# Optimization experiments

Measured on AMD Instinct MI355X. Metric: run time of the kernel, lower is better.

Reference implementation:

```python
import jax, jax.numpy as jnp
import numpy as np

N = 4096  # num_dev == num_task (required by elementwise msg computation)
D = 64    # embed_dim


def setup_inputs() -> dict:
    key = jax.random.key(0)
    ks = jax.random.split(key, 10)
    return {
        "embed": jax.random.normal(ks[0], (2 * N, D), jnp.float32),
        "adj_collab": jnp.zeros((N, N), jnp.float32),   # only .shape[0] is used
        "adj_interact": jnp.zeros((N, N), jnp.float32),  # unused in forward body
        "adj_similar": jnp.zeros((N, N), jnp.float32),   # unused in forward body
        "collab_score": jax.random.normal(ks[1], (N, N), jnp.float32),
        "interact_score": jax.random.normal(ks[2], (N, N), jnp.float32),
        "similar_score": jax.random.normal(ks[3], (N, N), jnp.float32),
        "deg_dev": jax.random.uniform(ks[4], (N,), jnp.float32, 1.0, 100.0),
        "deg_task": jax.random.uniform(ks[5], (N,), jnp.float32, 1.0, 100.0),
        "W1": jax.random.normal(ks[6], (D, D), jnp.float32) / np.sqrt(D).astype(np.float32),
        "b1": jnp.zeros((D,), jnp.float32),
        "W2": jax.random.normal(ks[7], (D, D), jnp.float32) / np.sqrt(D).astype(np.float32),
        "b2": jnp.zeros((D,), jnp.float32),
        "W3": jax.random.normal(ks[8], (D, D), jnp.float32) / np.sqrt(D).astype(np.float32),
        "b3": jnp.zeros((D,), jnp.float32),
    }


def _linear(x, W, b):
    # torch nn.Linear: x @ W.T + b
    return x @ W.T + b


def _calc_attention(src, dst, rel_score, src_deg, dst_deg):
    # msg = dst + src*dst ; per-row dot <src, msg> ; degree + sqrt(d) scaling ; softmax
    msg = dst + src * dst                      # [N, D]
    dot = jnp.sum(src * msg, axis=-1)          # [N]
    scale = dot / (jnp.sqrt(src_deg * dst_deg + 1e-8) * jnp.sqrt(jnp.float32(src.shape[-1])))
    att = jax.nn.softmax(rel_score * scale, axis=-1)  # [N, N] (scale broadcasts over columns)
    return att, msg


def reference(embed, adj_collab, adj_interact, adj_similar,
              collab_score, interact_score, similar_score,
              deg_dev, deg_task, W1, b1, W2, b2, W3, b3):
    num_dev = adj_collab.shape[0]
    dev = embed[:num_dev]       # [N, D]
    task = embed[num_dev:]      # [N, D]

    collab_att, collab_msg = _calc_attention(dev, dev, collab_score, deg_dev, deg_dev)
    collab_prop = collab_att @ _linear(collab_msg, W1, b1)

    interact_att, interact_msg = _calc_attention(dev, task, interact_score, deg_dev, deg_task)
    interact_prop = interact_att @ _linear(interact_msg, W2, b2)

    dev_prop = jax.nn.leaky_relu(_linear(dev + collab_prop + interact_prop, W3, b3), 0.2)

    similar_att, _similar_msg = _calc_attention(task, task, similar_score, deg_task, deg_task)
    similar_prop = similar_att @ _linear(task, W3, b3)  # note: original uses W3(task_embed), not the msg
    task_prop = jax.nn.leaky_relu(_linear(task + similar_prop, W3, b3), 0.2)

    # dropout omitted (eval mode / identity)
    return jnp.concatenate([dev_prop, task_prop], axis=0)
```

## Files before the change

### kernel.cpp

```cpp
#include <hip/hip_runtime.h>
#include <math.h>

#define N 4096
#define D 64
#define NSLICE 8
#define JLEN 512
#define CH 32
#define NCHUNK 16
#define SH 44.0f

#define S_OFF   0
#define MT_OFF  24576
#define E_OFF   32768
#define SCL_OFF 36864
#define LDS_BYTES 38912

typedef short bf16x8 __attribute__((ext_vector_type(8)));
typedef float f32x4  __attribute__((ext_vector_type(4)));

__device__ __forceinline__ unsigned short f2bf(float x) {
    unsigned int u = __float_as_uint(x);
    u += 0x7FFFu + ((u >> 16) & 1u);
    return (unsigned short)(u >> 16);
}
__device__ __forceinline__ float bf2f(unsigned short h) {
    return __uint_as_float(((unsigned int)h) << 16);
}

__device__ __forceinline__ void gld16(const void* g, void* l) {
    __builtin_amdgcn_global_load_lds(
        (const __attribute__((address_space(1))) void*)g,
        (__attribute__((address_space(3))) void*)l,
        16, 0, 0);
}

__device__ __forceinline__ void lds_barrier() {
    asm volatile("s_waitcnt lgkmcnt(0)" ::: "memory");
    __builtin_amdgcn_s_barrier();
    asm volatile("" ::: "memory");
}
__device__ __forceinline__ void plain_barrier() {
    asm volatile("" ::: "memory");
    __builtin_amdgcn_s_barrier();
    asm volatile("" ::: "memory");
}

__global__ __launch_bounds__(256) void prep_kernel(
    const float* __restrict__ embed,
    const float* __restrict__ degd, const float* __restrict__ degt,
    const float* __restrict__ W1, const float* __restrict__ b1,
    const float* __restrict__ W2, const float* __restrict__ b2,
    const float* __restrict__ W3, const float* __restrict__ b3,
    float* __restrict__ scale, unsigned short* __restrict__ Mt)
{
    const int rel = blockIdx.y;
    const float* W  = (rel == 0) ? W1 : (rel == 1 ? W2 : W3);
    const float* bb = (rel == 0) ? b1 : (rel == 1 ? b2 : b3);
    __shared__ float Wl[D][D + 1];
    __shared__ float xr[4][D];
    __shared__ unsigned short ot[4][D];
    const int tid = threadIdx.x;
    for (int idx = tid; idx < D * D; idx += 256)
        Wl[idx >> 6][idx & 63] = W[idx];
    const int w = tid >> 6, d = tid & 63;
    const int i0 = blockIdx.x * 4;
    const int i = i0 + w;

    float msg, term, xsrc, dga, dgb;
    if (rel == 0) {
        float s = embed[(size_t)i * D + d];
        msg = s + s * s; term = s * msg; xsrc = msg;
        dga = degd[i]; dgb = degd[i];
    } else if (rel == 1) {
        float s = embed[(size_t)i * D + d];
        float t = embed[(size_t)(N + i) * D + d];
        msg = t + s * t; term = s * msg; xsrc = msg;
        dga = degd[i]; dgb = degt[i];
    } else {
        float t = embed[(size_t)(N + i) * D + d];
        msg = t + t * t; term = t * msg; xsrc = t;
        dga = degt[i]; dgb = degt[i];
    }
    float dot = term;
    #pragma unroll
    for (int mm = 1; mm < 64; mm <<= 1) dot += __shfl_xor(dot, mm);
    if (d == 0)
        scale[rel * N + i] = dot / (sqrtf(dga * dgb + 1e-8f) * 8.0f);

    xr[w][d] = xsrc;
    __syncthreads();
    float o = bb[d];
    #pragma unroll 8
    for (int k = 0; k < D; ++k) o += xr[w][k] * Wl[d][k];
    ot[w][d] = f2bf(o);
    __syncthreads();
    if (tid < 64) {
        union { unsigned short h[4]; uint2 v; } t;
        t.h[0] = ot[0][tid]; t.h[1] = ot[1][tid];
        t.h[2] = ot[2][tid]; t.h[3] = ot[3][tid];
        *(uint2*)&Mt[((size_t)rel * D + tid) * N + i0] = t.v;
    }
}

__global__ __launch_bounds__(256, 4) void attn_kernel(
    const float* __restrict__ S0, const float* __restrict__ S1, const float* __restrict__ S2,
    const float* __restrict__ scale, const unsigned short* __restrict__ Mt,
    unsigned short* __restrict__ Up, float* __restrict__ lp)
{
    __shared__ __align__(16) char LDS[LDS_BYTES];
    const int rg = blockIdx.x, rel = blockIdx.y, sl = blockIdx.z;
    const float* S = (rel == 0) ? S0 : (rel == 1 ? S1 : S2);
    const unsigned short* Mtr = Mt + (size_t)rel * D * N;
    const int tid = threadIdx.x;
    const int lane = tid & 63, wave = tid >> 6;
    const int row = tid >> 2, q = tid & 3;
    const int j0 = sl * JLEN;

    const int srow = tid >> 3, sslot = tid & 7;
    const int sx = (sslot ^ (srow & 7)) * 4;
    const float* s0p = S + (size_t)(rg * 64 + srow) * N + j0 + sx;
    const float* s1p = S + (size_t)(rg * 64 + 32 + srow) * N + j0 + sx;
    const unsigned short* mtp = Mtr + (size_t)lane * N + j0 + wave * 8;
    char* sldsw = LDS + S_OFF + wave * 1024;
    char* mldsw = LDS + MT_OFF + wave * 1024;

#define ISSUE_S(cc, bb) do {                                       \
        gld16(s0p + (cc) * CH, sldsw + (bb) * 8192);               \
        gld16(s1p + (cc) * CH, sldsw + (bb) * 8192 + 4096);        \
    } while (0)
#define ISSUE_M(cc, bb) gld16(mtp + (cc) * CH, mldsw + (bb) * 4096)

    {
        const f32x4 sc0 = *(const f32x4*)(scale + rel * N + j0 + tid * 2 - (tid & 1) * 4 + (tid & 1) * 4);
        (void)sc0;
    }
    for (int k = tid; k < JLEN; k += 256)
        *(float*)(LDS + SCL_OFF + k * 4) = scale[rel * N + j0 + k];
    asm volatile("" ::: "memory");
    ISSUE_M(0, 0);
    ISSUE_S(0, 0);
    ISSUE_S(1, 1);
    lds_barrier();

    const int wbase = wave * 16;
    const int lrow  = lane & 15;
    const int lk    = lane >> 4;
    float l = 0.f;
    f32x4 acc[4];
    #pragma unroll
    for (int ct = 0; ct < 4; ++ct) {
        acc[ct][0] = 0.f; acc[ct][1] = 0.f; acc[ct][2] = 0.f; acc[ct][3] = 0.f;
    }

    #pragma unroll
    for (int c = 0; c < NCHUNK; ++c) {
        if (c < NCHUNK - 1) asm volatile("s_waitcnt vmcnt(2)" ::: "memory");
        else                asm volatile("s_waitcnt vmcnt(0)" ::: "memory");
        plain_barrier();

        if (c + 1 < NCHUNK) ISSUE_M(c + 1, (c + 1) & 1);
        if (c + 2 < NCHUNK) { int t = c + 2; int b = t % 3; ISSUE_S(t, b); }

        {
            const char* sb = LDS + S_OFF + (c % 3) * 8192 + row * 128;
            const int r7 = row & 7;
            const f32x4 sa = *(const f32x4*)(sb + (((2 * q)     ^ r7) << 4));
            const f32x4 sc = *(const f32x4*)(sb + (((2 * q + 1) ^ r7) << 4));
            const char* cb = LDS + SCL_OFF + c * 128 + q * 32;
            const f32x4 ca = *(const f32x4*)(cb);
            const f32x4 cc = *(const f32x4*)(cb + 16);
            float e[8];
            #pragma unroll
            for (int u = 0; u < 4; ++u) {
                e[u]     = __expf(fmaf(sa[u], ca[u], -SH));
                e[4 + u] = __expf(fmaf(sc[u], cc[u], -SH));
            }
            #pragma unroll
            for (int k = 0; k < 8; ++k) l += e[k];
            union { unsigned short h[8]; uint4 v; } pk;
            #pragma unroll
            for (int k = 0; k < 8; ++k) pk.h[k] = f2bf(e[k]);
            *(uint4*)(LDS + E_OFF + q * 1024 + ((row ^ q) << 4)) = pk.v;
        }

        lds_barrier();

        __builtin_amdgcn_s_setprio(1);
        {
            const char* mb = LDS + MT_OFF + (c & 1) * 4096 + lk * 1024;
            const bf16x8 a = *(const bf16x8*)(
                LDS + E_OFF + lk * 1024 + (((wbase + lrow) ^ lk) << 4));
            #pragma unroll
            for (int ct = 0; ct < 4; ++ct) {
                const bf16x8 b = *(const bf16x8*)(mb + ((ct * 16 + lrow) << 4));
                acc[ct] = __builtin_amdgcn_mfma_f32_16x16x32_bf16(a, b, acc[ct], 0, 0, 0);
            }
        }
        __builtin_amdgcn_s_setprio(0);
    }
#undef ISSUE_S
#undef ISSUE_M

    unsigned short* R = (unsigned short*)LDS;
    #pragma unroll
    for (int ct = 0; ct < 4; ++ct)
        #pragma unroll
        for (int r = 0; r < 4; ++r) {
            const int ri = wbase + lk * 4 + r;
            R[ri * 64 + ct * 16 + lrow] = f2bf(acc[ct][r]);
        }
    lds_barrier();
    const size_t pbase = (size_t)((rel * 64 + rg) * NSLICE + sl);
    unsigned short* up = Up + pbase * 4096;
    {
        const uint4* src = (const uint4*)R;
        uint4*       dst = (uint4*)up;
        dst[tid]       = src[tid];
        dst[256 + tid] = src[256 + tid];
    }
    l += __shfl_xor(l, 1);
    l += __shfl_xor(l, 2);
    if (q == 0) lp[pbase * 64 + row] = l;
}

__device__ __forceinline__ float combine_row(
    const unsigned short* __restrict__ Up, const float* __restrict__ lp,
    int rel, int i, int d)
{
    const int rg = i >> 6, r = i & 63;
    const int base = (rel * 64 + rg) * NSLICE;
    float lt = 0.f, u = 0.f;
    #pragma unroll
    for (int p = 0; p < NSLICE; ++p) {
        lt += lp[(base + p) * 64 + r];
        u  += bf2f(Up[(size_t)(base + p) * 4096 + r * 64 + d]);
    }
    return u / lt;
}

__global__ __launch_bounds__(256) void final_kernel(
    const float* __restrict__ embed,
    const unsigned short* __restrict__ Up, const float* __restrict__ lp,
    const float* __restrict__ W3, const float* __restrict__ b3,
    float* __restrict__ out)
{
    __shared__ float Wl[D][D + 1];
    __shared__ float xs[4][D];
    const int tid = threadIdx.x;
    for (int idx = tid; idx < D * D; idx += 256)
        Wl[idx >> 6][idx & 63] = W3[idx];
    const int w = tid >> 6, d = tid & 63;
    const int g = blockIdx.x * 4 + w;

    float x = embed[(size_t)g * D + d];
    if (g < N) {
        x += combine_row(Up, lp, 0, g, d);
        x += combine_row(Up, lp, 1, g, d);
    } else {
        x += combine_row(Up, lp, 2, g - N, d);
    }
    xs[w][d] = x;
    __syncthreads();
    float o = b3[d];
    #pragma unroll 8
    for (int k = 0; k < D; ++k) o += xs[w][k] * Wl[d][k];
    o = (o > 0.f) ? o : 0.2f * o;
    out[(size_t)g * D + d] = o;
}

extern "C" void kernel_launch(void* const* d_in, const int* in_sizes, int n_in,
                              void* d_out, int out_size, void* d_ws, size_t ws_size,
                              hipStream_t stream)
{
    const float* embed = (const float*)d_in[0];
    const float* Sc   = (const float*)d_in[4];
    const float* Si   = (const float*)d_in[5];
    const float* Ss   = (const float*)d_in[6];
    const float* degd = (const float*)d_in[7];
    const float* degt = (const float*)d_in[8];
    const float* W1 = (const float*)d_in[9];
    const float* b1 = (const float*)d_in[10];
    const float* W2 = (const float*)d_in[11];
    const float* b2 = (const float*)d_in[12];
    const float* W3 = (const float*)d_in[13];
    const float* b3 = (const float*)d_in[14];
    float* out = (float*)d_out;

    float* ws    = (float*)d_ws;
    float* scale = ws;
    float* lp    = ws + 12288;
    unsigned short* Mt = (unsigned short*)(lp + 98304);
    unsigned short* Up = Mt + 786432;

    prep_kernel<<<dim3(N / 4, 3), 256, 0, stream>>>(
        embed, degd, degt, W1, b1, W2, b2, W3, b3, scale, Mt);
    attn_kernel<<<dim3(64, 3, NSLICE), 256, 0, stream>>>(
        Sc, Si, Ss, scale, Mt, Up, lp);
    final_kernel<<<dim3(2 * N / 4), 256, 0, stream>>>(
        embed, Up, lp, W3, b3, out);
}
```

Before: 61.77 us.

## Process 128 score rows per attention block to reuse each M tile twice

```diff
diff --git a/kernel.cpp b/kernel.cpp
--- a/kernel.cpp
+++ b/kernel.cpp
@@ -3,6 +3,7 @@
 
 #define N 4096
 #define D 64
+#define ROWS 128
 #define NSLICE 8
 #define JLEN 512
 #define CH 32
@@ -10,10 +11,10 @@
 #define SH 44.0f
 
 #define S_OFF   0
-#define MT_OFF  24576
-#define E_OFF   32768
-#define SCL_OFF 36864
-#define LDS_BYTES 38912
+#define MT_OFF  32768
+#define E_OFF   40960
+#define SCL_OFF 49152
+#define LDS_BYTES 51200
 
 typedef short bf16x8 __attribute__((ext_vector_type(8)));
 typedef float f32x4  __attribute__((ext_vector_type(4)));
@@ -102,7 +103,7 @@
     }
 }
 
-__global__ __launch_bounds__(256, 4) void attn_kernel(
+__global__ __launch_bounds__(256, 3) void attn_kernel(
     const float* __restrict__ S0, const float* __restrict__ S1, const float* __restrict__ S2,
     const float* __restrict__ scale, const unsigned short* __restrict__ Mt,
     unsigned short* __restrict__ Up, float* __restrict__ lp)
@@ -113,127 +114,140 @@
     const unsigned short* Mtr = Mt + (size_t)rel * D * N;
     const int tid = threadIdx.x;
     const int lane = tid & 63, wave = tid >> 6;
-    const int row = tid >> 2, q = tid & 3;
+    const int row = tid >> 1, q = tid & 1;
     const int j0 = sl * JLEN;
 
-    const int srow = tid >> 3, sslot = tid & 7;
-    const int sx = (sslot ^ (srow & 7)) * 4;
-    const float* s0p = S + (size_t)(rg * 64 + srow) * N + j0 + sx;
-    const float* s1p = S + (size_t)(rg * 64 + 32 + srow) * N + j0 + sx;
+    const int sr8 = lane >> 3, sslot = lane & 7;
+    const int sgx = (sslot ^ sr8) * 4;
+    const float* spb = S + (size_t)(rg * ROWS + wave * 32 + sr8) * N + j0 + sgx;
     const unsigned short* mtp = Mtr + (size_t)lane * N + j0 + wave * 8;
-    char* sldsw = LDS + S_OFF + wave * 1024;
+    char* sldsw = LDS + S_OFF + wave * 4096;
     char* mldsw = LDS + MT_OFF + wave * 1024;
 
-#define ISSUE_S(cc, bb) do {                                       \
-        gld16(s0p + (cc) * CH, sldsw + (bb) * 8192);               \
-        gld16(s1p + (cc) * CH, sldsw + (bb) * 8192 + 4096);        \
+#define ISSUE_S(cc, bb) do {                                                   \
+        gld16(spb + (size_t)0 * 8 * N + (cc) * CH, sldsw + (bb) * 16384);      \
+        gld16(spb + (size_t)1 * 8 * N + (cc) * CH, sldsw + (bb) * 16384 + 1024); \
+        gld16(spb + (size_t)2 * 8 * N + (cc) * CH, sldsw + (bb) * 16384 + 2048); \
+        gld16(spb + (size_t)3 * 8 * N + (cc) * CH, sldsw + (bb) * 16384 + 3072); \
     } while (0)
 #define ISSUE_M(cc, bb) gld16(mtp + (cc) * CH, mldsw + (bb) * 4096)
 
-    {
-        const f32x4 sc0 = *(const f32x4*)(scale + rel * N + j0 + tid * 2 - (tid & 1) * 4 + (tid & 1) * 4);
-        (void)sc0;
-    }
     for (int k = tid; k < JLEN; k += 256)
         *(float*)(LDS + SCL_OFF + k * 4) = scale[rel * N + j0 + k];
     asm volatile("" ::: "memory");
+    ISSUE_S(0, 0);
     ISSUE_M(0, 0);
-    ISSUE_S(0, 0);
     ISSUE_S(1, 1);
     lds_barrier();
 
-    const int wbase = wave * 16;
-    const int lrow  = lane & 15;
-    const int lk    = lane >> 4;
+    const int lrow = lane & 15;
+    const int lk   = lane >> 4;
     float l = 0.f;
-    f32x4 acc[4];
-    #pragma unroll
-    for (int ct = 0; ct < 4; ++ct) {
-        acc[ct][0] = 0.f; acc[ct][1] = 0.f; acc[ct][2] = 0.f; acc[ct][3] = 0.f;
-    }
+    f32x4 acc[2][4];
+    #pragma unroll
+    for (int t = 0; t < 2; ++t)
+        #pragma unroll
+        for (int ct = 0; ct < 4; ++ct) {
+            acc[t][ct][0] = 0.f; acc[t][ct][1] = 0.f;
+            acc[t][ct][2] = 0.f; acc[t][ct][3] = 0.f;
+        }
 
     #pragma unroll
     for (int c = 0; c < NCHUNK; ++c) {
-        if (c < NCHUNK - 1) asm volatile("s_waitcnt vmcnt(2)" ::: "memory");
+        if (c < NCHUNK - 1) asm volatile("s_waitcnt vmcnt(4)" ::: "memory");
         else                asm volatile("s_waitcnt vmcnt(0)" ::: "memory");
         plain_barrier();
 
         if (c + 1 < NCHUNK) ISSUE_M(c + 1, (c + 1) & 1);
-        if (c + 2 < NCHUNK) { int t = c + 2; int b = t % 3; ISSUE_S(t, b); }
 
         {
-            const char* sb = LDS + S_OFF + (c % 3) * 8192 + row * 128;
+            const char* sb = LDS + S_OFF + (c & 1) * 16384 + row * 128;
             const int r7 = row & 7;
-            const f32x4 sa = *(const f32x4*)(sb + (((2 * q)     ^ r7) << 4));
-            const f32x4 sc = *(const f32x4*)(sb + (((2 * q + 1) ^ r7) << 4));
-            const char* cb = LDS + SCL_OFF + c * 128 + q * 32;
-            const f32x4 ca = *(const f32x4*)(cb);
-            const f32x4 cc = *(const f32x4*)(cb + 16);
-            float e[8];
+            const f32x4 s0 = *(const f32x4*)(sb + (((q * 4 + 0) ^ r7) << 4));
+            const f32x4 s1 = *(const f32x4*)(sb + (((q * 4 + 1) ^ r7) << 4));
+            const f32x4 s2 = *(const f32x4*)(sb + (((q * 4 + 2) ^ r7) << 4));
+            const f32x4 s3 = *(const f32x4*)(sb + (((q * 4 + 3) ^ r7) << 4));
+            const char* cb = LDS + SCL_OFF + c * 128 + q * 64;
+            const f32x4 c0 = *(const f32x4*)(cb);
+            const f32x4 c1 = *(const f32x4*)(cb + 16);
+            const f32x4 c2 = *(const f32x4*)(cb + 32);
+            const f32x4 c3 = *(const f32x4*)(cb + 48);
+            float e[16];
             #pragma unroll
             for (int u = 0; u < 4; ++u) {
-                e[u]     = __expf(fmaf(sa[u], ca[u], -SH));
-                e[4 + u] = __expf(fmaf(sc[u], cc[u], -SH));
+                e[u]      = __expf(fmaf(s0[u], c0[u], -SH));
+                e[4 + u]  = __expf(fmaf(s1[u], c1[u], -SH));
+                e[8 + u]  = __expf(fmaf(s2[u], c2[u], -SH));
+                e[12 + u] = __expf(fmaf(s3[u], c3[u], -SH));
             }
             #pragma unroll
-            for (int k = 0; k < 8; ++k) l += e[k];
-            union { unsigned short h[8]; uint4 v; } pk;
-            #pragma unroll
-            for (int k = 0; k < 8; ++k) pk.h[k] = f2bf(e[k]);
-            *(uint4*)(LDS + E_OFF + q * 1024 + ((row ^ q) << 4)) = pk.v;
+            for (int k = 0; k < 16; ++k) l += e[k];
+            union { unsigned short h[8]; uint4 v; } p0, p1;
+            #pragma unroll
+            for (int k = 0; k < 8; ++k) { p0.h[k] = f2bf(e[k]); p1.h[k] = f2bf(e[8 + k]); }
+            const int kgA = 2 * q, kgB = 2 * q + 1;
+            *(uint4*)(LDS + E_OFF + kgA * 2048 + ((row ^ (2 * kgA)) << 4)) = p0.v;
+            *(uint4*)(LDS + E_OFF + kgB * 2048 + ((row ^ (2 * kgB)) << 4)) = p1.v;
         }
 
         lds_barrier();
 
-        __builtin_amdgcn_s_setprio(1);
+        if (c + 2 < NCHUNK) ISSUE_S(c + 2, c & 1);
+
         {
             const char* mb = LDS + MT_OFF + (c & 1) * 4096 + lk * 1024;
-            const bf16x8 a = *(const bf16x8*)(
-                LDS + E_OFF + lk * 1024 + (((wbase + lrow) ^ lk) << 4));
+            const int ra0 = wave * 32 + lrow, ra1 = wave * 32 + 16 + lrow;
+            const bf16x8 a0 = *(const bf16x8*)(
+                LDS + E_OFF + lk * 2048 + ((ra0 ^ (2 * lk)) << 4));
+            const bf16x8 a1 = *(const bf16x8*)(
+                LDS + E_OFF + lk * 2048 + ((ra1 ^ (2 * lk)) << 4));
             #pragma unroll
             for (int ct = 0; ct < 4; ++ct) {
                 const bf16x8 b = *(const bf16x8*)(mb + ((ct * 16 + lrow) << 4));
-                acc[ct] = __builtin_amdgcn_mfma_f32_16x16x32_bf16(a, b, acc[ct], 0, 0, 0);
+                acc[0][ct] = __builtin_amdgcn_mfma_f32_16x16x32_bf16(a0, b, acc[0][ct], 0, 0, 0);
+                acc[1][ct] = __builtin_amdgcn_mfma_f32_16x16x32_bf16(a1, b, acc[1][ct], 0, 0, 0);
             }
         }
-        __builtin_amdgcn_s_setprio(0);
     }
 #undef ISSUE_S
 #undef ISSUE_M
 
     unsigned short* R = (unsigned short*)LDS;
     #pragma unroll
-    for (int ct = 0; ct < 4; ++ct)
+    for (int t = 0; t < 2; ++t)
         #pragma unroll
-        for (int r = 0; r < 4; ++r) {
-            const int ri = wbase + lk * 4 + r;
-            R[ri * 64 + ct * 16 + lrow] = f2bf(acc[ct][r]);
-        }
+        for (int ct = 0; ct < 4; ++ct)
+            #pragma unroll
+            for (int r = 0; r < 4; ++r) {
+                const int ri = wave * 32 + t * 16 + lk * 4 + r;
+                R[ri * 64 + ct * 16 + lrow] = f2bf(acc[t][ct][r]);
+            }
     lds_barrier();
-    const size_t pbase = (size_t)((rel * 64 + rg) * NSLICE + sl);
-    unsigned short* up = Up + pbase * 4096;
+    const size_t pbase = (size_t)((rel * 32 + rg) * NSLICE + sl);
+    unsigned short* up = Up + pbase * 8192;
     {
         const uint4* src = (const uint4*)R;
         uint4*       dst = (uint4*)up;
         dst[tid]       = src[tid];
         dst[256 + tid] = src[256 + tid];
+        dst[512 + tid] = src[512 + tid];
+        dst[768 + tid] = src[768 + tid];
     }
     l += __shfl_xor(l, 1);
-    l += __shfl_xor(l, 2);
-    if (q == 0) lp[pbase * 64 + row] = l;
+    if (q == 0) lp[pbase * ROWS + row] = l;
 }
 
 __device__ __forceinline__ float combine_row(
     const unsigned short* __restrict__ Up, const float* __restrict__ lp,
     int rel, int i, int d)
 {
-    const int rg = i >> 6, r = i & 63;
-    const int base = (rel * 64 + rg) * NSLICE;
+    const int rt = i >> 7, r = i & 127;
+    const int base = (rel * 32 + rt) * NSLICE;
     float lt = 0.f, u = 0.f;
     #pragma unroll
     for (int p = 0; p < NSLICE; ++p) {
-        lt += lp[(base + p) * 64 + r];
-        u  += bf2f(Up[(size_t)(base + p) * 4096 + r * 64 + d]);
+        lt += lp[(base + p) * ROWS + r];
+        u  += bf2f(Up[(size_t)(base + p) * 8192 + r * 64 + d]);
     }
     return u / lt;
 }
@@ -294,7 +308,7 @@
 
     prep_kernel<<<dim3(N / 4, 3), 256, 0, stream>>>(
         embed, degd, degt, W1, b1, W2, b2, W3, b3, scale, Mt);
-    attn_kernel<<<dim3(64, 3, NSLICE), 256, 0, stream>>>(
+    attn_kernel<<<dim3(N / ROWS, 3, NSLICE), 256, 0, stream>>>(
         Sc, Si, Ss, scale, Mt, Up, lp);
     final_kernel<<<dim3(2 * N / 4), 256, 0, stream>>>(
         embed, Up, lp, W3, b3, out);
```

After: 58.98 us. 4.5% less time.
